# Performance work log

Measured on AMD Instinct MI355X. Metric: run time of the kernel, lower is better.

The kernel has to match this reference:

```python
import jax, jax.numpy as jnp
import numpy as np

NUM_HEADS = 6
ATTN_TH = 0.0
NEG_INF = -10000.0  # masked-score fill for threshold pruning


def setup_inputs() -> dict:
    key = jax.random.key(0)
    k1, k2, k3 = jax.random.split(key, 3)
    B, N, C = 8, 1024, 384
    x = jax.random.normal(k1, (B, N, C), dtype=jnp.float32)
    # Linear weights (torch layout: [out, in]), scaled like default init
    w_qkv = jax.random.normal(k2, (3 * C, C), dtype=jnp.float32) * (1.0 / np.sqrt(C))
    b_qkv = jnp.zeros((3 * C,), dtype=jnp.float32)
    w_proj = jax.random.normal(k3, (C, C), dtype=jnp.float32) * (1.0 / np.sqrt(C))
    b_proj = jnp.zeros((C,), dtype=jnp.float32)
    return {"x": x, "w_qkv": w_qkv, "b_qkv": b_qkv, "w_proj": w_proj, "b_proj": b_proj}


def reference(x, w_qkv, b_qkv, w_proj, b_proj):
    B, N, C = x.shape
    H = NUM_HEADS
    D = C // H
    scale = D ** -0.5
    # QAct nodes are identity (quant=False); QLinear is a plain linear.
    qkv = jnp.einsum('bnc,oc->bno', x, w_qkv) + b_qkv          # [B,N,3C]
    qkv = qkv.reshape(B, N, 3, H, D).transpose(2, 0, 3, 1, 4)   # [3,B,H,N,D]
    q, k, v = qkv[0], qkv[1], qkv[2]
    attn = jnp.einsum('bhnd,bhmd->bhnm', q, k) * scale          # [B,H,N,N]
    # Threshold pruning: scores below Attn_Th are masked out of the softmax.
    attn = jnp.where(attn < ATTN_TH, NEG_INF, attn)
    attn = jax.nn.softmax(attn, axis=-1)
    out = jnp.einsum('bhnm,bhmd->bhnd', attn, v)                # [B,H,N,D]
    out = out.transpose(0, 2, 1, 3).reshape(B, N, C)
    out = jnp.einsum('bnc,oc->bno', out, w_proj) + b_proj
    return out
```

## Files before the change

### kernel.cpp

```cpp
#include <hip/hip_runtime.h>
#include <hip/hip_bf16.h>


typedef __attribute__((__ext_vector_type__(8))) __bf16 bf16x8;
typedef __attribute__((__ext_vector_type__(8))) unsigned short ushort8;
typedef __attribute__((__ext_vector_type__(4))) unsigned short ushort4v;
typedef __attribute__((__ext_vector_type__(4))) short short4v;
typedef __attribute__((__ext_vector_type__(4))) float f32x4;

#define NX 3145728
#define NQ 442368
#define NP 147456

#define QSCALE 0.1803368801111204f

__device__ __forceinline__ f32x4 mfma32(bf16x8 a, bf16x8 b, f32x4 c) {
    return __builtin_amdgcn_mfma_f32_16x16x32_bf16(a, b, c, 0, 0, 0);
}
__device__ __forceinline__ f32x4 mfma16(short4v a, short4v b, f32x4 c) {
    return __builtin_amdgcn_mfma_f32_16x16x16bf16_1k(a, b, c, 0, 0, 0);
}

__device__ __forceinline__ unsigned short f2bf(float f) {
    union { float f; unsigned int i; } x; x.f = f;
    unsigned int u = x.i;
    return (unsigned short)((u + 0x7fffu + ((u >> 16) & 1u)) >> 16);
}

__device__ __forceinline__ unsigned cvtpk(float a, float b) {
    unsigned r;
    asm("v_cvt_pk_bf16_f32 %0, %1, %2" : "=v"(r) : "v"(a), "v"(b));
    return r;
}

__device__ __forceinline__ void dma16(const unsigned short* g, unsigned short* l) {
    __builtin_amdgcn_global_load_lds(
        (const __attribute__((address_space(1))) unsigned int*)g,
        (__attribute__((address_space(3))) unsigned int*)l, 16, 0, 0);
}

__global__ __launch_bounds__(256) void cvt_bf16(
    const float* __restrict__ x, const float* __restrict__ wq, const float* __restrict__ wp,
    unsigned short* __restrict__ xb, unsigned short* __restrict__ wqb, unsigned short* __restrict__ wpb)
{
    int i = blockIdx.x * 256 + threadIdx.x;
    const float* src; unsigned short* dst; int off;
    if (i < NX / 4)              { src = x;  dst = xb;  off = i * 4; }
    else if (i < (NX + NQ) / 4)  { src = wq; dst = wqb; off = i * 4 - NX; }
    else                         { src = wp; dst = wpb; off = i * 4 - NX - NQ; }
    float4 v = *(const float4*)(src + off);
    ushort4v r;
    r[0] = f2bf(v.x); r[1] = f2bf(v.y); r[2] = f2bf(v.z); r[3] = f2bf(v.w);
    *(ushort4v*)(dst + off) = r;
}

template <int MODE, int TM>
__global__ __launch_bounds__(TM * 2) void gemm_bt(
    const unsigned short* __restrict__ A,
    const unsigned short* __restrict__ B,
    const float* __restrict__ bias,
    unsigned short* __restrict__ qg,
    unsigned short* __restrict__ kg,
    unsigned short* __restrict__ vg,
    float* __restrict__ out,
    int M, int N, int K)
{
    const int tid  = threadIdx.x;
    const int lane = tid & 63;
    const int wave = tid >> 6;
    const int l15  = lane & 15;
    const int quad = lane >> 4;
    const int m0 = blockIdx.x * TM;
    const int n0 = blockIdx.y * 128;
    const int wm = (wave >> 1) * 64;
    const int wn = (wave & 1) * 64;

    __shared__ __align__(16) unsigned short As[2 * TM * 32];
    __shared__ __align__(16) unsigned short Bs[2 * 128 * 32];

    f32x4 acc[4][4];
    #pragma unroll
    for (int i = 0; i < 4; ++i)
        #pragma unroll
        for (int j = 0; j < 4; ++j)
            acc[i][j] = (f32x4){0.f, 0.f, 0.f, 0.f};

    auto stage = [&](int k0, int buf) {
        #pragma unroll
        for (int t = 0; t < 2; ++t) {
            int i = tid + t * TM * 2;
            dma16(A + (size_t)(m0 + (i >> 2)) * K + k0 + (i & 3) * 8,
                  As + buf * TM * 32 + t * TM * 16 + wave * 512);
        }
        #pragma unroll
        for (int t = 0; t < 512 / (TM * 2); ++t) {
            int i = tid + t * TM * 2;
            dma16(B + (size_t)(n0 + (i >> 2)) * K + k0 + (i & 3) * 8,
                  Bs + buf * 4096 + t * TM * 16 + wave * 512);
        }
    };

    const int nk = K >> 5;
    stage(0, 0);
    for (int ki = 0; ki < nk; ++ki) {
        __syncthreads();
        if (ki + 1 < nk) stage((ki + 1) << 5, (ki + 1) & 1);
        const unsigned short* as = As + (ki & 1) * TM * 32;
        const unsigned short* bs = Bs + (ki & 1) * 4096;

        bf16x8 af[4], bff[4];
        #pragma unroll
        for (int mt = 0; mt < 4; ++mt)
            af[mt] = *(const bf16x8*)(as + (wm + mt * 16 + l15) * 32 + quad * 8);
        #pragma unroll
        for (int nt = 0; nt < 4; ++nt)
            bff[nt] = *(const bf16x8*)(bs + (wn + nt * 16 + l15) * 32 + quad * 8);
        #pragma unroll
        for (int mt = 0; mt < 4; ++mt)
            #pragma unroll
            for (int nt = 0; nt < 4; ++nt)
                acc[mt][nt] = mfma32(af[mt], bff[nt], acc[mt][nt]);
    }

    if constexpr (MODE == 0) {
        if (n0 < 384) {
            #pragma unroll
            for (int nt = 0; nt < 4; ++nt) {
                int n = n0 + wn + nt * 16 + l15;
                float bv = bias[n];
                #pragma unroll
                for (int mt = 0; mt < 4; ++mt) {
                    int mbase = m0 + wm + mt * 16 + quad * 4;
                    #pragma unroll
                    for (int r = 0; r < 4; ++r)
                        qg[(size_t)(mbase + r) * 384 + n] = f2bf((acc[mt][nt][r] + bv) * QSCALE);
                }
            }
        } else if (n0 < 768) {
            #pragma unroll
            for (int nt = 0; nt < 4; ++nt) {
                int n = n0 + wn + nt * 16 + l15;
                float bv = bias[n];
                int c2 = n - 384;
                int h = c2 >> 6, ck = c2 & 63;
                int half = ck >> 5, qd = (ck >> 3) & 3, j = ck & 7;
                #pragma unroll
                for (int mt = 0; mt < 4; ++mt) {
                    int mbase = m0 + wm + mt * 16 + quad * 4;
                    #pragma unroll
                    for (int r = 0; r < 4; ++r) {
                        int tok = mbase + r;
                        int b = tok >> 10, kv = tok & 1023;
                        int kt = kv >> 4, lk = kv & 15;
                        kg[(size_t)(b * 6 + h) * 65536 +
                           ((((size_t)kt * 2 + half) * 4 + qd) * 16 + lk) * 8 + j]
                            = f2bf(acc[mt][nt][r] + bv);
                    }
                }
            }
        } else {
            #pragma unroll
            for (int nt = 0; nt < 4; ++nt) {
                int n = n0 + wn + nt * 16 + l15;
                float bv = bias[n];
                int c2 = n - 768;
                int h = c2 >> 6, d = c2 & 63;
                int dt = d >> 4, lv = d & 15;
                #pragma unroll
                for (int mt = 0; mt < 4; ++mt) {
                    int mbase = m0 + wm + mt * 16 + quad * 4;
                    int b = mbase >> 10, kvb = mbase & 1023;
                    int cc = kvb >> 6, jt = (kvb >> 4) & 3, qd = (kvb >> 2) & 3;
                    ushort4v pk;
                    #pragma unroll
                    for (int r = 0; r < 4; ++r) pk[r] = f2bf(acc[mt][nt][r] + bv);
                    *(ushort4v*)(vg + (size_t)(b * 6 + h) * 65536 + (size_t)cc * 4096 +
                                 (((jt * 4 + dt) * 4 + qd) * 16 + lv) * 4) = pk;
                }
            }
        }
    } else {
        #pragma unroll
        for (int nt = 0; nt < 4; ++nt) {
            int n = n0 + wn + nt * 16 + l15;
            float bv = bias[n];
            #pragma unroll
            for (int mt = 0; mt < 4; ++mt) {
                int mbase = m0 + wm + mt * 16 + quad * 4;
                #pragma unroll
                for (int r = 0; r < 4; ++r)
                    out[(size_t)(mbase + r) * N + n] = acc[mt][nt][r] + bv;
            }
        }
    }
}

__global__ __launch_bounds__(256) void attn_fused(
    const unsigned short* __restrict__ qg,
    const unsigned short* __restrict__ kg,
    const unsigned short* __restrict__ vg,
    unsigned short* __restrict__ aout)
{
    const int tid  = threadIdx.x;
    const int wave = tid >> 6;
    const int lane = tid & 63;
    const int l15  = lane & 15;
    const int quad = lane >> 4;
    const int id = blockIdx.x;
    const int s  = id % 48;
    const int qt = id / 48;
    const int b  = s / 6;
    const int h  = s % 6;

    const size_t rowbase = (size_t)b * 1024;
    const unsigned short* Kslab = kg + (size_t)s * 65536;
    const unsigned short* Vslab = vg + (size_t)s * 65536;
    const int q0 = qt * 64 + wave * 16;

    __shared__ __align__(16) unsigned short Kb[2 * 4096];
    __shared__ __align__(16) unsigned short Vb[2 * 4096];

    bf16x8 aq0, aq1;
    {
        const unsigned short* qrow = qg + (rowbase + q0 + l15) * 384 + h * 64 + quad * 8;
        aq0 = *(const bf16x8*)qrow;
        aq1 = *(const bf16x8*)(qrow + 32);
    }

    const short4v ONES4 = (short4v){(short)0x3F80, (short)0x3F80, (short)0x3F80, (short)0x3F80};

    f32x4 accO[4];
    #pragma unroll
    for (int dt = 0; dt < 4; ++dt) accO[dt] = (f32x4){0.f, 0.f, 0.f, 0.f};
    f32x4 accS = (f32x4){0.f, 0.f, 0.f, 0.f};

    auto stage = [&](int c, int buf) {
        #pragma unroll
        for (int t = 0; t < 2; ++t) {
            int i = tid + t * 256;
            dma16(Kslab + (size_t)c * 4096 + i * 8, Kb + buf * 4096 + t * 2048 + wave * 512);
            dma16(Vslab + (size_t)c * 4096 + i * 8, Vb + buf * 4096 + t * 2048 + wave * 512);
        }
    };

    stage(0, 0);
    for (int c = 0; c < 16; ++c) {
        __syncthreads();
        if (c + 1 < 16) stage(c + 1, (c + 1) & 1);
        const unsigned short* kb = Kb + (c & 1) * 4096;
        const unsigned short* vb = Vb + (c & 1) * 4096;

        #pragma unroll
        for (int kt = 0; kt < 4; ++kt) {
            bf16x8 ka = *(const bf16x8*)(kb + (((kt * 2 + 0) * 4 + quad) * 16 + l15) * 8);
            bf16x8 kbf = *(const bf16x8*)(kb + (((kt * 2 + 1) * 4 + quad) * 16 + l15) * 8);
            f32x4 z = (f32x4){0.f, 0.f, 0.f, 0.f};
            z = mfma32(ka, aq0, z);
            z = mfma32(kbf, aq1, z);

            float e0 = __builtin_amdgcn_exp2f(z[0]); e0 = (z[0] < 0.f) ? 0.f : e0;
            float e1 = __builtin_amdgcn_exp2f(z[1]); e1 = (z[1] < 0.f) ? 0.f : e1;
            float e2 = __builtin_amdgcn_exp2f(z[2]); e2 = (z[2] < 0.f) ? 0.f : e2;
            float e3 = __builtin_amdgcn_exp2f(z[3]); e3 = (z[3] < 0.f) ? 0.f : e3;

            union { unsigned u[2]; short4v s; } pp;
            pp.u[0] = cvtpk(e0, e1);
            pp.u[1] = cvtpk(e2, e3);
            short4v p = pp.s;

            accS = mfma16(ONES4, p, accS);
            #pragma unroll
            for (int dt = 0; dt < 4; ++dt) {
                short4v vv = *(const short4v*)(vb + (((kt * 4 + dt) * 4 + quad) * 16 + l15) * 4);
                accO[dt] = mfma16(vv, p, accO[dt]);
            }
        }
    }

    float inv = 1.0f / accS[0];

    unsigned short* orow = aout + (rowbase + q0 + l15) * 384 + h * 64 + quad * 4;
    #pragma unroll
    for (int dt = 0; dt < 4; ++dt) {
        union { unsigned u[2]; ushort4v s; } pk;
        pk.u[0] = cvtpk(accO[dt][0] * inv, accO[dt][1] * inv);
        pk.u[1] = cvtpk(accO[dt][2] * inv, accO[dt][3] * inv);
        *(ushort4v*)(orow + dt * 16) = pk.s;
    }
}

extern "C" void kernel_launch(void* const* d_in, const int* in_sizes, int n_in,
                              void* d_out, int out_size, void* d_ws, size_t ws_size,
                              hipStream_t stream) {
    const float* x      = (const float*)d_in[0];
    const float* w_qkv  = (const float*)d_in[1];
    const float* b_qkv  = (const float*)d_in[2];
    const float* w_proj = (const float*)d_in[3];
    const float* b_proj = (const float*)d_in[4];
    float* out = (float*)d_out;

    unsigned short* qg   = (unsigned short*)d_ws;
    unsigned short* kgp  = qg   + (size_t)NX;
    unsigned short* vgp  = kgp  + (size_t)NX;
    unsigned short* aout = vgp  + (size_t)NX;
    unsigned short* xb   = aout + (size_t)NX;
    unsigned short* wqb  = xb   + (size_t)NX;
    unsigned short* wpb  = wqb  + (size_t)NQ;

    cvt_bf16<<<3648, 256, 0, stream>>>(x, w_qkv, w_proj, xb, wqb, wpb);
    gemm_bt<0, 256><<<dim3(32, 9), 512, 0, stream>>>(
        xb, wqb, b_qkv, qg, kgp, vgp, nullptr, 8192, 1152, 384);
    attn_fused<<<768, 256, 0, stream>>>(qg, kgp, vgp, aout);
    gemm_bt<1, 64><<<dim3(128, 3), 128, 0, stream>>>(
        aout, wpb, b_proj, nullptr, nullptr, nullptr, out, 8192, 384, 384);
}
```

Measured before the change: 124.0 us.

## Use 16x16x32 MFMA for PV by pairing score tiles via lane shuffles

The attention inner loop now computes two 16-key score tiles at a time and exchanges half of the packed probabilities between lanes with a cross-lane shuffle. This forms the 8-element bf16 operands needed by the 16x16x32 MFMA for the PV and row-sum products, replacing the 16x16x16 instructions. The V layout written by the QKV GEMM epilogue is changed to match the new operand pattern. This halves the PV/sum MFMA count and widens the LDS reads, at the cost of two shuffles per pair of tiles and more complex index math in the epilogue.

```diff
diff --git a/kernel.cpp b/kernel.cpp
--- a/kernel.cpp
+++ b/kernel.cpp
@@ -16,9 +16,6 @@
 
 __device__ __forceinline__ f32x4 mfma32(bf16x8 a, bf16x8 b, f32x4 c) {
     return __builtin_amdgcn_mfma_f32_16x16x32_bf16(a, b, c, 0, 0, 0);
-}
-__device__ __forceinline__ f32x4 mfma16(short4v a, short4v b, f32x4 c) {
-    return __builtin_amdgcn_mfma_f32_16x16x16bf16_1k(a, b, c, 0, 0, 0);
 }
 
 __device__ __forceinline__ unsigned short f2bf(float f) {
@@ -170,12 +167,21 @@
                 for (int mt = 0; mt < 4; ++mt) {
                     int mbase = m0 + wm + mt * 16 + quad * 4;
                     int b = mbase >> 10, kvb = mbase & 1023;
-                    int cc = kvb >> 6, jt = (kvb >> 4) & 3, qd = (kvb >> 2) & 3;
+                    int cc = kvb >> 6;
+                    int hh = (kvb >> 5) & 1;
+                    int rem2 = kvb & 31;
+                    int qv, j;
+                    if (rem2 < 16) { qv = (rem2 >> 3) << 1; j = rem2 & 7; }
+                    else {
+                        int m2 = rem2 - 16;
+                        qv = 1 + ((m2 >> 3) << 1);
+                        j = (((m2 >> 2) & 1) ^ 1) << 2;
+                    }
                     ushort4v pk;
                     #pragma unroll
                     for (int r = 0; r < 4; ++r) pk[r] = f2bf(acc[mt][nt][r] + bv);
-                    *(ushort4v*)(vg + (size_t)(b * 6 + h) * 65536 + (size_t)cc * 4096 +
-                                 (((jt * 4 + dt) * 4 + qd) * 16 + lv) * 4) = pk;
+                    *(ushort4v*)(vg + (size_t)(b * 6 + h) * 65536 +
+                                 ((((size_t)cc * 2 + hh) * 4 + dt) * 4 + qv) * 128 + lv * 8 + j) = pk;
                 }
             }
         }
@@ -227,7 +233,10 @@
         aq1 = *(const bf16x8*)(qrow + 32);
     }
 
-    const short4v ONES4 = (short4v){(short)0x3F80, (short)0x3F80, (short)0x3F80, (short)0x3F80};
+    union { unsigned short us[8]; bf16x8 v; } ones_u;
+    #pragma unroll
+    for (int i = 0; i < 8; ++i) ones_u.us[i] = 0x3F80;
+    const bf16x8 ONES8 = ones_u.v;
 
     f32x4 accO[4];
     #pragma unroll
@@ -242,6 +251,8 @@
             dma16(Vslab + (size_t)c * 4096 + i * 8, Vb + buf * 4096 + t * 2048 + wave * 512);
         }
     };
+
+    const bool oddq = (quad & 1) != 0;
 
     stage(0, 0);
     for (int c = 0; c < 16; ++c) {
@@ -251,28 +262,43 @@
         const unsigned short* vb = Vb + (c & 1) * 4096;
 
         #pragma unroll
-        for (int kt = 0; kt < 4; ++kt) {
-            bf16x8 ka = *(const bf16x8*)(kb + (((kt * 2 + 0) * 4 + quad) * 16 + l15) * 8);
-            bf16x8 kbf = *(const bf16x8*)(kb + (((kt * 2 + 1) * 4 + quad) * 16 + l15) * 8);
-            f32x4 z = (f32x4){0.f, 0.f, 0.f, 0.f};
-            z = mfma32(ka, aq0, z);
-            z = mfma32(kbf, aq1, z);
-
-            float e0 = __builtin_amdgcn_exp2f(z[0]); e0 = (z[0] < 0.f) ? 0.f : e0;
-            float e1 = __builtin_amdgcn_exp2f(z[1]); e1 = (z[1] < 0.f) ? 0.f : e1;
-            float e2 = __builtin_amdgcn_exp2f(z[2]); e2 = (z[2] < 0.f) ? 0.f : e2;
-            float e3 = __builtin_amdgcn_exp2f(z[3]); e3 = (z[3] < 0.f) ? 0.f : e3;
-
-            union { unsigned u[2]; short4v s; } pp;
-            pp.u[0] = cvtpk(e0, e1);
-            pp.u[1] = cvtpk(e2, e3);
-            short4v p = pp.s;
-
-            accS = mfma16(ONES4, p, accS);
+        for (int hh = 0; hh < 2; ++hh) {
+            bf16x8 ka0 = *(const bf16x8*)(kb + (((4 * hh + 0) * 4 + quad) * 16 + l15) * 8);
+            bf16x8 ka1 = *(const bf16x8*)(kb + (((4 * hh + 1) * 4 + quad) * 16 + l15) * 8);
+            f32x4 za = (f32x4){0.f, 0.f, 0.f, 0.f};
+            za = mfma32(ka0, aq0, za);
+            za = mfma32(ka1, aq1, za);
+            bf16x8 kb0 = *(const bf16x8*)(kb + (((4 * hh + 2) * 4 + quad) * 16 + l15) * 8);
+            bf16x8 kb1 = *(const bf16x8*)(kb + (((4 * hh + 3) * 4 + quad) * 16 + l15) * 8);
+            f32x4 zb = (f32x4){0.f, 0.f, 0.f, 0.f};
+            zb = mfma32(kb0, aq0, zb);
+            zb = mfma32(kb1, aq1, zb);
+
+            float ea0 = __builtin_amdgcn_exp2f(za[0]); ea0 = (za[0] < 0.f) ? 0.f : ea0;
+            float ea1 = __builtin_amdgcn_exp2f(za[1]); ea1 = (za[1] < 0.f) ? 0.f : ea1;
+            float ea2 = __builtin_amdgcn_exp2f(za[2]); ea2 = (za[2] < 0.f) ? 0.f : ea2;
+            float ea3 = __builtin_amdgcn_exp2f(za[3]); ea3 = (za[3] < 0.f) ? 0.f : ea3;
+            float eb0 = __builtin_amdgcn_exp2f(zb[0]); eb0 = (zb[0] < 0.f) ? 0.f : eb0;
+            float eb1 = __builtin_amdgcn_exp2f(zb[1]); eb1 = (zb[1] < 0.f) ? 0.f : eb1;
+            float eb2 = __builtin_amdgcn_exp2f(zb[2]); eb2 = (zb[2] < 0.f) ? 0.f : eb2;
+            float eb3 = __builtin_amdgcn_exp2f(zb[3]); eb3 = (zb[3] < 0.f) ? 0.f : eb3;
+
+            unsigned A0 = cvtpk(ea0, ea1), A1 = cvtpk(ea2, ea3);
+            unsigned B0 = cvtpk(eb0, eb1), B1 = cvtpk(eb2, eb3);
+
+            unsigned send0 = oddq ? A0 : B0, send1 = oddq ? A1 : B1;
+            unsigned keep0 = oddq ? B0 : A0, keep1 = oddq ? B1 : A1;
+            unsigned rr0 = (unsigned)__shfl_xor((int)send0, 16, 64);
+            unsigned rr1 = (unsigned)__shfl_xor((int)send1, 16, 64);
+
+            union { unsigned u[4]; bf16x8 v; } pw;
+            pw.u[0] = keep0; pw.u[1] = keep1; pw.u[2] = rr0; pw.u[3] = rr1;
+
+            accS = mfma32(ONES8, pw.v, accS);
             #pragma unroll
             for (int dt = 0; dt < 4; ++dt) {
-                short4v vv = *(const short4v*)(vb + (((kt * 4 + dt) * 4 + quad) * 16 + l15) * 4);
-                accO[dt] = mfma16(vv, p, accO[dt]);
+                bf16x8 vv = *(const bf16x8*)(vb + (((hh * 4 + dt) * 4 + quad) * 16 + l15) * 8);
+                accO[dt] = mfma32(vv, pw.v, accO[dt]);
             }
         }
     }
```

Result: slower. 127.4 us (+2.8%).

## Load K/V fragments directly from global into registers, double-buffered, dropping LDS staging

Applied to the files above, without the earlier changes.

Replaces the LDS double-buffered DMA staging of K and V tiles, along with its per-chunk __syncthreads, with direct global-to-register fragment loads. Two fragments are register double-buffered so each load overlaps compute on the other fragment. This removes the barriers and LDS traffic. In exchange, each of the four waves in a block now fetches the same K/V data separately from global/L2, and register pressure rises.

```diff
diff --git a/kernel.cpp b/kernel.cpp
--- a/kernel.cpp
+++ b/kernel.cpp
@@ -213,12 +213,10 @@
     const int h  = s % 6;
 
     const size_t rowbase = (size_t)b * 1024;
-    const unsigned short* Kslab = kg + (size_t)s * 65536;
-    const unsigned short* Vslab = vg + (size_t)s * 65536;
     const int q0 = qt * 64 + wave * 16;
 
-    __shared__ __align__(16) unsigned short Kb[2 * 4096];
-    __shared__ __align__(16) unsigned short Vb[2 * 4096];
+    const unsigned short* Kbase = kg + (size_t)s * 65536 + (quad * 16 + l15) * 8;
+    const unsigned short* Vbase = vg + (size_t)s * 65536 + (quad * 16 + l15) * 4;
 
     bf16x8 aq0, aq1;
     {
@@ -234,58 +232,82 @@
     for (int dt = 0; dt < 4; ++dt) accO[dt] = (f32x4){0.f, 0.f, 0.f, 0.f};
     f32x4 accS = (f32x4){0.f, 0.f, 0.f, 0.f};
 
-    auto stage = [&](int c, int buf) {
-        #pragma unroll
-        for (int t = 0; t < 2; ++t) {
-            int i = tid + t * 256;
-            dma16(Kslab + (size_t)c * 4096 + i * 8, Kb + buf * 4096 + t * 2048 + wave * 512);
-            dma16(Vslab + (size_t)c * 4096 + i * 8, Vb + buf * 4096 + t * 2048 + wave * 512);
-        }
+    struct Frag {
+        bf16x8 k0, k1, k2, k3;
+        short4v v0, v1, v2, v3, v4, v5, v6, v7;
     };
 
-    stage(0, 0);
-    for (int c = 0; c < 16; ++c) {
-        __syncthreads();
-        if (c + 1 < 16) stage(c + 1, (c + 1) & 1);
-        const unsigned short* kb = Kb + (c & 1) * 4096;
-        const unsigned short* vb = Vb + (c & 1) * 4096;
-
-        #pragma unroll
-        for (int kt = 0; kt < 4; ++kt) {
-            bf16x8 ka = *(const bf16x8*)(kb + (((kt * 2 + 0) * 4 + quad) * 16 + l15) * 8);
-            bf16x8 kbf = *(const bf16x8*)(kb + (((kt * 2 + 1) * 4 + quad) * 16 + l15) * 8);
-            f32x4 z = (f32x4){0.f, 0.f, 0.f, 0.f};
-            z = mfma32(ka, aq0, z);
-            z = mfma32(kbf, aq1, z);
-
-            float e0 = __builtin_amdgcn_exp2f(z[0]); e0 = (z[0] < 0.f) ? 0.f : e0;
-            float e1 = __builtin_amdgcn_exp2f(z[1]); e1 = (z[1] < 0.f) ? 0.f : e1;
-            float e2 = __builtin_amdgcn_exp2f(z[2]); e2 = (z[2] < 0.f) ? 0.f : e2;
-            float e3 = __builtin_amdgcn_exp2f(z[3]); e3 = (z[3] < 0.f) ? 0.f : e3;
-
-            union { unsigned u[2]; short4v s; } pp;
-            pp.u[0] = cvtpk(e0, e1);
-            pp.u[1] = cvtpk(e2, e3);
-            short4v p = pp.s;
-
-            accS = mfma16(ONES4, p, accS);
-            #pragma unroll
-            for (int dt = 0; dt < 4; ++dt) {
-                short4v vv = *(const short4v*)(vb + (((kt * 4 + dt) * 4 + quad) * 16 + l15) * 4);
-                accO[dt] = mfma16(vv, p, accO[dt]);
-            }
-        }
-    }
+    auto loadf = [&](int st, Frag& f) {
+        const unsigned short* kp = Kbase + st * 2048;
+        f.k0 = *(const bf16x8*)(kp);
+        f.k1 = *(const bf16x8*)(kp + 512);
+        f.k2 = *(const bf16x8*)(kp + 1024);
+        f.k3 = *(const bf16x8*)(kp + 1536);
+        const unsigned short* vp = Vbase + (st >> 1) * 4096 + (st & 1) * 2048;
+        f.v0 = *(const short4v*)(vp);
+        f.v1 = *(const short4v*)(vp + 256);
+        f.v2 = *(const short4v*)(vp + 512);
+        f.v3 = *(const short4v*)(vp + 768);
+        f.v4 = *(const short4v*)(vp + 1024);
+        f.v5 = *(const short4v*)(vp + 1280);
+        f.v6 = *(const short4v*)(vp + 1536);
+        f.v7 = *(const short4v*)(vp + 1792);
+    };
+
+    auto computef = [&](const Frag& f) {
+        f32x4 za = (f32x4){0.f, 0.f, 0.f, 0.f};
+        za = mfma32(f.k0, aq0, za);
+        za = mfma32(f.k1, aq1, za);
+        f32x4 zb = (f32x4){0.f, 0.f, 0.f, 0.f};
+        zb = mfma32(f.k2, aq0, zb);
+        zb = mfma32(f.k3, aq1, zb);
+
+        float ea0 = __builtin_amdgcn_exp2f(za[0]); ea0 = (za[0] < 0.f) ? 0.f : ea0;
+        float ea1 = __builtin_amdgcn_exp2f(za[1]); ea1 = (za[1] < 0.f) ? 0.f : ea1;
+        float ea2 = __builtin_amdgcn_exp2f(za[2]); ea2 = (za[2] < 0.f) ? 0.f : ea2;
+        float ea3 = __builtin_amdgcn_exp2f(za[3]); ea3 = (za[3] < 0.f) ? 0.f : ea3;
+        float eb0 = __builtin_amdgcn_exp2f(zb[0]); eb0 = (zb[0] < 0.f) ? 0.f : eb0;
+        float eb1 = __builtin_amdgcn_exp2f(zb[1]); eb1 = (zb[1] < 0.f) ? 0.f : eb1;
+        float eb2 = __builtin_amdgcn_exp2f(zb[2]); eb2 = (zb[2] < 0.f) ? 0.f : eb2;
+        float eb3 = __builtin_amdgcn_exp2f(zb[3]); eb3 = (zb[3] < 0.f) ? 0.f : eb3;
+
+        union { unsigned u[2]; short4v s4; } pa, pb;
+        pa.u[0] = cvtpk(ea0, ea1); pa.u[1] = cvtpk(ea2, ea3);
+        pb.u[0] = cvtpk(eb0, eb1); pb.u[1] = cvtpk(eb2, eb3);
+
+        accS = mfma16(ONES4, pa.s4, accS);
+        accS = mfma16(ONES4, pb.s4, accS);
+        accO[0] = mfma16(f.v0, pa.s4, accO[0]);
+        accO[1] = mfma16(f.v1, pa.s4, accO[1]);
+        accO[2] = mfma16(f.v2, pa.s4, accO[2]);
+        accO[3] = mfma16(f.v3, pa.s4, accO[3]);
+        accO[0] = mfma16(f.v4, pb.s4, accO[0]);
+        accO[1] = mfma16(f.v5, pb.s4, accO[1]);
+        accO[2] = mfma16(f.v6, pb.s4, accO[2]);
+        accO[3] = mfma16(f.v7, pb.s4, accO[3]);
+    };
+
+    Frag fA, fB;
+    loadf(0, fA);
+    loadf(1, fB);
+    for (int it = 0; it < 15; ++it) {
+        computef(fA);
+        loadf(2 * it + 2, fA);
+        computef(fB);
+        loadf(2 * it + 3, fB);
+    }
+    computef(fA);
+    computef(fB);
 
     float inv = 1.0f / accS[0];
 
     unsigned short* orow = aout + (rowbase + q0 + l15) * 384 + h * 64 + quad * 4;
     #pragma unroll
     for (int dt = 0; dt < 4; ++dt) {
-        union { unsigned u[2]; ushort4v s; } pk;
+        union { unsigned u[2]; ushort4v s4; } pk;
         pk.u[0] = cvtpk(accO[dt][0] * inv, accO[dt][1] * inv);
         pk.u[1] = cvtpk(accO[dt][2] * inv, accO[dt][3] * inv);
-        *(ushort4v*)(orow + dt * 16) = pk.s;
+        *(ushort4v*)(orow + dt * 16) = pk.s4;
     }
 }
 
```

Measured after the change: 138.3 us. 11.6% more time.
